# Kernel tuning notes

Measured on AMD Instinct MI355X. Metric: run time of the kernel, lower is better.

Reference implementation:

```python
import jax, jax.numpy as jnp
import numpy as np

B, H, W, DIM = 32, 56, 56, 512
WS, SHIFT, HEADS, MLP = 7, 3, 16, 2048
S = WS * WS
NW = (H // WS) * (W // WS)


def _rel_pos_index():
    coords = np.stack(np.meshgrid(np.arange(WS), np.arange(WS), indexing='ij')).reshape(2, -1)
    rel = (coords[:, :, None] - coords[:, None, :]).transpose(1, 2, 0)
    rel[:, :, 0] += WS - 1
    rel[:, :, 1] += WS - 1
    rel[:, :, 0] *= 2 * WS - 1
    return rel.sum(-1)  # [S, S] ints in [0, 169)


def _attn_mask():
    mask = np.zeros((H, W))
    cnt = 0
    sls = (slice(0, -WS), slice(-WS, -SHIFT), slice(-SHIFT, None))
    for hs in sls:
        for ws in sls:
            mask[hs, ws] = cnt
            cnt += 1
    mw = mask.reshape(H // WS, WS, W // WS, WS).transpose(0, 2, 1, 3).reshape(-1, S)
    am = mw[:, None, :] - mw[:, :, None]
    return np.where(am != 0, -100.0, 0.0).astype(np.float32)  # [NW, S, S]


_RPI = jnp.asarray(_rel_pos_index().reshape(-1))
_MASK = jnp.asarray(_attn_mask())


def setup_inputs() -> dict:
    key = jax.random.key(0)
    ks = jax.random.split(key, 6)
    sc = lambda fan: 1.0 / np.sqrt(fan)
    return {
        'x': jax.random.normal(ks[0], (B, H * W, DIM), jnp.float32),
        'qkv_w': jax.random.normal(ks[1], (DIM, 3 * DIM), jnp.float32) * sc(DIM),
        'qkv_b': jnp.zeros((3 * DIM,), jnp.float32),
        'proj_w': jax.random.normal(ks[2], (DIM, DIM), jnp.float32) * sc(DIM),
        'proj_b': jnp.zeros((DIM,), jnp.float32),
        'rel_bias': jax.random.normal(ks[3], (169, HEADS), jnp.float32) * 0.02,
        'norm1_g': jnp.ones((DIM,), jnp.float32),
        'norm1_b': jnp.zeros((DIM,), jnp.float32),
        'norm2_g': jnp.ones((DIM,), jnp.float32),
        'norm2_b': jnp.zeros((DIM,), jnp.float32),
        'mlp_w1': jax.random.normal(ks[4], (DIM, MLP), jnp.float32) * sc(DIM),
        'mlp_b1': jnp.zeros((MLP,), jnp.float32),
        'mlp_w2': jax.random.normal(ks[5], (MLP, DIM), jnp.float32) * sc(MLP),
        'mlp_b2': jnp.zeros((DIM,), jnp.float32),
    }


def _ln(z, g, b):
    m = z.mean(-1, keepdims=True)
    v = z.var(-1, keepdims=True)
    return (z - m) * jax.lax.rsqrt(v + 1e-5) * g + b


def reference(x, qkv_w, qkv_b, proj_w, proj_b, rel_bias,
              norm1_g, norm1_b, norm2_g, norm2_b,
              mlp_w1, mlp_b1, mlp_w2, mlp_b2):
    hd = DIM // HEADS
    scale = hd ** -0.5
    skip = x
    h = _ln(x, norm1_g, norm1_b).reshape(B, H, W, DIM)
    h = jnp.roll(h, (-SHIFT, -SHIFT), axis=(1, 2))
    # window partition -> [B*NW, S, DIM]
    win = h.reshape(B, H // WS, WS, W // WS, WS, DIM).transpose(0, 1, 3, 2, 4, 5).reshape(-1, S, DIM)
    qkv = (win @ qkv_w + qkv_b).reshape(-1, S, 3, HEADS, hd).transpose(2, 0, 3, 1, 4)
    q, k, v = qkv[0] * scale, qkv[1], qkv[2]
    attn = jnp.einsum('whqd,whkd->whqk', q, k)  # [B*NW, HEADS, S, S]
    bias = rel_bias[_RPI].reshape(S, S, HEADS).transpose(2, 0, 1)
    attn = attn + bias[None]
    attn = attn.reshape(B, NW, HEADS, S, S) + _MASK[None, :, None]
    attn = jax.nn.softmax(attn.reshape(-1, HEADS, S, S), axis=-1)
    out = jnp.einsum('whqk,whkd->whqd', attn, v).transpose(0, 2, 1, 3).reshape(-1, S, DIM)
    out = out @ proj_w + proj_b
    # window reverse + unshift
    out = out.reshape(B, H // WS, W // WS, WS, WS, DIM).transpose(0, 1, 3, 2, 4, 5).reshape(B, H, W, DIM)
    out = jnp.roll(out, (SHIFT, SHIFT), axis=(1, 2)).reshape(B, H * W, DIM)
    x1 = skip + out
    h2 = _ln(x1, norm2_g, norm2_b)
    h2 = jax.nn.gelu(h2 @ mlp_w1 + mlp_b1, approximate=False) @ mlp_w2 + mlp_b2
    return x1 + h2
```

## Files before the change

### kernel.cpp

```cpp
#include <hip/hip_runtime.h>
#include <hip/hip_bf16.h>
#include <math.h>

#define BB 32
#define HH 56
#define WWD 56
#define DIM 512
#define WSZ 7
#define SHIFT 3
#define HEADS 16
#define MLPD 2048
#define SS 49
#define NWIN 64
#define HD 32
#define TOK (BB*HH*WWD)
#define NQKV 1536

typedef __hip_bfloat16 bf16;
typedef __attribute__((ext_vector_type(8))) short short8;
typedef __attribute__((ext_vector_type(4))) float floatx4;

__device__ __forceinline__ float bf2f(bf16 v){ return __bfloat162float(v); }
__device__ __forceinline__ bf16  f2bf(float v){ return __float2bfloat16(v); }
__device__ __forceinline__ float rd_ext(const void* p, size_t i, int fp32){
    return fp32 ? ((const float*)p)[i] : bf2f(((const bf16*)p)[i]);
}
__device__ __forceinline__ void gload16(const bf16* g, bf16* l){
    __builtin_amdgcn_global_load_lds(
        (const __attribute__((address_space(1))) void*)g,
        (__attribute__((address_space(3))) void*)l, 16, 0, 0);
}

__global__ void sniff_kernel(const unsigned short* __restrict__ x, int* __restrict__ flag)
{
    int lane = threadIdx.x;
    int insane = 0;
    #pragma unroll
    for (int t = 0; t < 2; t++){
        unsigned short u = x[2*(lane + t*64)];
        int e = (u >> 7) & 0xFF;
        if (e < 100 || e > 133) insane++;
    }
    #pragma unroll
    for (int m = 1; m < 64; m <<= 1) insane += __shfl_xor(insane, m);
    if (lane == 0) *flag = (insane > 64) ? 1 : 0;
}

template<int MODE>
__global__ __launch_bounds__(256) void ln_kernel(const void* __restrict__ xv,
        const void* __restrict__ g, const void* __restrict__ bvec,
        bf16* __restrict__ out, const int* __restrict__ flagp)
{
    const int fp32 = *flagp;
    int token = blockIdx.x * 4 + (threadIdx.x >> 6);
    int lane  = threadIdx.x & 63;
    float f[8];
    if (MODE == 0 && fp32){
        const float* xr = (const float*)xv + (size_t)token*DIM + lane*8;
        float4 a = *(const float4*)xr;
        float4 b = *(const float4*)(xr + 4);
        f[0]=a.x; f[1]=a.y; f[2]=a.z; f[3]=a.w;
        f[4]=b.x; f[5]=b.y; f[6]=b.z; f[7]=b.w;
    } else {
        uint4 v = *((const uint4*)((const bf16*)xv + (size_t)token * DIM) + lane);
        bf16 e[8]; *(uint4*)e = v;
        #pragma unroll
        for (int i = 0; i < 8; i++) f[i] = bf2f(e[i]);
    }
    float sum = 0.f, ssq = 0.f;
    #pragma unroll
    for (int i = 0; i < 8; i++){ sum += f[i]; ssq += f[i]*f[i]; }
    #pragma unroll
    for (int m = 1; m < 64; m <<= 1){ sum += __shfl_xor(sum, m); ssq += __shfl_xor(ssq, m); }
    float mean = sum * (1.0f/DIM);
    float var  = ssq * (1.0f/DIM) - mean*mean;
    float rstd = rsqrtf(var + 1e-5f);
    bf16 o[8];
    #pragma unroll
    for (int i = 0; i < 8; i++){
        float gv = rd_ext(g,    lane*8+i, fp32);
        float bv = rd_ext(bvec, lane*8+i, fp32);
        o[i] = f2bf((f[i]-mean)*rstd*gv + bv);
    }
    size_t drow;
    if (MODE == 0){
        int bidx = token / (HH*WWD);
        int t    = token % (HH*WWD);
        int hs = t / WWD, wsrc = t % WWD;
        int i2 = (hs  + HH  - SHIFT) % HH;
        int j2 = (wsrc+ WWD - SHIFT) % WWD;
        int wh = i2 / WSZ, ii = i2 % WSZ;
        int ww = j2 / WSZ, jj = j2 % WSZ;
        int wi = bidx*NWIN + wh*8 + ww;
        drow = (size_t)wi*SS + ii*WSZ + jj;
    } else {
        drow = token;
    }
    *((uint4*)(out + drow*DIM) + lane) = *(uint4*)o;
}

__global__ void cvt_transpose(const void* __restrict__ in, bf16* __restrict__ out,
                              int K, int N, const int* __restrict__ flagp)
{
    const int fp32 = *flagp;
    int id = blockIdx.x*256 + threadIdx.x;
    if (id >= K*N) return;
    int k = id / N, n = id - k*N;
    out[(size_t)n*K + k] = f2bf(rd_ext(in, id, fp32));
}

__global__ void stab_kernel(const void* __restrict__ rel_bias,
                            float* __restrict__ stab, const int* __restrict__ flagp)
{
    const int fp32 = *flagp;
    int idx = blockIdx.x*256 + threadIdx.x;
    int h   = idx / (4*64*52);
    int rem = idx - h*(4*64*52);
    int cls = rem / (64*52);
    int rem2= rem - cls*(64*52);
    int i   = rem2 / 52;
    int j   = rem2 - i*52;
    float v = 0.f;
    if (i < SS && j < SS){
        int qi = i/7, qj = i - qi*7;
        int ki = j/7, kj = j - ki*7;
        int rpi = (qi-ki+6)*13 + (qj-kj+6);
        v = rd_ext(rel_bias, (size_t)rpi*HEADS + h, fp32);
        int ri = ((cls&2) ? (qi<4?1:2) : 0)*3 + ((cls&1) ? (qj<4?1:2) : 0);
        int rj = ((cls&2) ? (ki<4?1:2) : 0)*3 + ((cls&1) ? (kj<4?1:2) : 0);
        if (ri != rj) v -= 100.0f;
    }
    stab[idx] = v;
}

__global__ __launch_bounds__(256, 2) void attn_kernel(
        const bf16* __restrict__ qkv, const float* __restrict__ stab,
        bf16* __restrict__ out)
{
    alignas(16) __shared__ bf16 Ps[4][64*72];
    const int tid  = threadIdx.x;
    const int wave = tid >> 6, lane = tid & 63;
    const int g = lane >> 4, l16 = lane & 15;
    const int job = blockIdx.x*4 + wave;
    const int wi = job >> 4, h = job & 15;
    const bf16* qbase = qkv + (size_t)wi*(SS*NQKV) + h*HD;

    short8 qf[4], kf[4];
    #pragma unroll
    for (int t = 0; t < 4; t++){
        int row = t*16 + l16;
        qf[t] = *(const short8*)(qbase + (size_t)row*NQKV +       g*8);
        kf[t] = *(const short8*)(qbase + (size_t)row*NQKV + 512 + g*8);
    }
    floatx4 st[4][4];
    #pragma unroll
    for (int mt = 0; mt < 4; mt++)
        #pragma unroll
        for (int nt = 0; nt < 4; nt++)
            st[mt][nt] = floatx4{0.f,0.f,0.f,0.f};
    #pragma unroll
    for (int mt = 0; mt < 4; mt++)
        #pragma unroll
        for (int nt = 0; nt < 4; nt++)
            st[mt][nt] = __builtin_amdgcn_mfma_f32_16x16x32_bf16(
                             kf[mt], qf[nt], st[mt][nt], 0, 0, 0);

    const int nw = wi & 63;
    const int cls = (((nw >> 3) == 7) ? 2 : 0) | (((nw & 7) == 7) ? 1 : 0);
    const float* tb = stab + (size_t)((h*4 + cls)*64)*52;
    bf16* pw = Ps[wave];
    #pragma unroll
    for (int nt = 0; nt < 4; nt++){
        const int i = nt*16 + l16;
        const float* trow = tb + i*52;
        float mx = -1e30f;
        #pragma unroll
        for (int mt = 0; mt < 4; mt++){
            float4 t4 = *(const float4*)(trow + mt*16 + g*4);
            #pragma unroll
            for (int r = 0; r < 4; r++){
                int j = mt*16 + g*4 + r;
                float v = st[mt][nt][r]*0.17677669529663687f + ((const float*)&t4)[r];
                v = (j < SS) ? v : -1e30f;
                st[mt][nt][r] = v;
                mx = fmaxf(mx, v);
            }
        }
        mx = fmaxf(mx, __shfl_xor(mx, 16));
        mx = fmaxf(mx, __shfl_xor(mx, 32));
        float sum = 0.f;
        #pragma unroll
        for (int mt = 0; mt < 4; mt++)
            #pragma unroll
            for (int r = 0; r < 4; r++){
                float e = __expf(st[mt][nt][r] - mx);
                st[mt][nt][r] = e;
                sum += e;
            }
        sum += __shfl_xor(sum, 16);
        sum += __shfl_xor(sum, 32);
        float inv = 1.0f / sum;
        #pragma unroll
        for (int mt = 0; mt < 4; mt++){
            union { bf16 e[4]; uint2 u; } pk;
            #pragma unroll
            for (int r = 0; r < 4; r++) pk.e[r] = f2bf(st[mt][nt][r]*inv);
            *(uint2*)(pw + i*72 + mt*16 + g*4) = pk.u;
        }
    }

    const unsigned short* vbase = (const unsigned short*)qkv
                                + (size_t)wi*(SS*NQKV) + 1024 + h*HD;
    short8 vf[2][2];
    #pragma unroll
    for (int md = 0; md < 2; md++){
        int d = md*16 + l16;
        #pragma unroll
        for (int kt = 0; kt < 2; kt++){
            short8 f;
            #pragma unroll
            for (int jj = 0; jj < 8; jj++){
                int j  = kt*32 + g*8 + jj;
                int jc = (j < SS) ? j : SS-1;
                unsigned short t = vbase[(size_t)jc*NQKV + d];
                f[jj] = (j < SS) ? (short)t : (short)0;
            }
            vf[md][kt] = f;
        }
    }

    floatx4 o[2][4];
    #pragma unroll
    for (int md = 0; md < 2; md++)
        #pragma unroll
        for (int nt = 0; nt < 4; nt++)
            o[md][nt] = floatx4{0.f,0.f,0.f,0.f};
    #pragma unroll
    for (int kt = 0; kt < 2; kt++){
        #pragma unroll
        for (int nt = 0; nt < 4; nt++){
            short8 pf = *(const short8*)(pw + (nt*16 + l16)*72 + kt*32 + g*8);
            #pragma unroll
            for (int md = 0; md < 2; md++)
                o[md][nt] = __builtin_amdgcn_mfma_f32_16x16x32_bf16(
                                vf[md][kt], pf, o[md][nt], 0, 0, 0);
        }
    }

    #pragma unroll
    for (int nt = 0; nt < 4; nt++){
        int i = nt*16 + l16;
        if (i < SS){
            #pragma unroll
            for (int md = 0; md < 2; md++){
                union { bf16 e[4]; uint2 u; } ob;
                #pragma unroll
                for (int r = 0; r < 4; r++) ob.e[r] = f2bf(o[md][nt][r]);
                *(uint2*)(out + ((size_t)wi*SS + i)*DIM + h*HD + md*16 + g*4) = ob.u;
            }
        }
    }
}

template<int NT, int KT, int EPI>
__global__ __launch_bounds__(256) void gemm_kernel(
    const bf16* __restrict__ A, const bf16* __restrict__ Bt,
    const void* __restrict__ bias, void* __restrict__ Cv,
    const void* __restrict__ extra, const int* __restrict__ flagp)
{
    alignas(16) __shared__ bf16 As[128*32];
    alignas(16) __shared__ bf16 Bs[128*32];
    const int fp32 = *flagp;
    const int tid = threadIdx.x;

    const int nxt = NT/128;
    const int bid = blockIdx.x + blockIdx.y*nxt;
    const int nwg = nxt*784;
    const int cpx = nwg >> 3;
    const int wid = (bid & 7)*cpx + (bid >> 3);
    const int m0 = (wid / nxt) * 128;
    const int n0 = (wid % nxt) * 128;

    const int wave = tid >> 6, lane = tid & 63;
    const int wm = wave & 1, wn = wave >> 1;
    const int qd = lane >> 4, l16 = lane & 15;
    const int lrow  = lane >> 2;
    const int lslot = lane & 3;

    floatx4 acc[4][4];
    #pragma unroll
    for (int i = 0; i < 4; i++)
        #pragma unroll
        for (int j = 0; j < 4; j++)
            acc[i][j] = floatx4{0.f,0.f,0.f,0.f};

    for (int kt = 0; kt < KT; kt += 32){
        #pragma unroll
        for (int r = 0; r < 2; r++){
            int chunk = wave + r*4;
            int row = chunk*16 + lrow;
            gload16(A  + (size_t)(m0+row)*KT + kt + lslot*8, As + chunk*512);
            gload16(Bt + (size_t)(n0+row)*KT + kt + lslot*8, Bs + chunk*512);
        }
        __syncthreads();
        short8 af[4], bfr[4];
        #pragma unroll
        for (int mt = 0; mt < 4; mt++)
            af[mt] = *(const short8*)(As + (wm*64 + mt*16 + l16)*32 + qd*8);
        #pragma unroll
        for (int nt = 0; nt < 4; nt++)
            bfr[nt] = *(const short8*)(Bs + (wn*64 + nt*16 + l16)*32 + qd*8);
        #pragma unroll
        for (int mt = 0; mt < 4; mt++)
            #pragma unroll
            for (int nt = 0; nt < 4; nt++)
                acc[mt][nt] = __builtin_amdgcn_mfma_f32_16x16x32_bf16(
                                  af[mt], bfr[nt], acc[mt][nt], 0, 0, 0);
        __syncthreads();
    }

    #pragma unroll
    for (int mt = 0; mt < 4; mt++){
        #pragma unroll
        for (int nt = 0; nt < 4; nt++){
            #pragma unroll
            for (int r = 0; r < 4; r++){
                int m = m0 + wm*64 + mt*16 + qd*4 + r;
                int n = n0 + wn*64 + nt*16 + l16;
                float val = acc[mt][nt][r] + rd_ext(bias, n, fp32);
                if (EPI == 1){
                    val = 0.5f * val * (1.0f + erff(val * 0.70710678118654752f));
                }
                if (EPI == 2){
                    int wi = m / SS, s = m % SS;
                    int b_ = wi >> 6, nw = wi & 63;
                    int hr = (nw >> 3)*WSZ + s / WSZ;
                    int wr = (nw & 7)*WSZ + s % WSZ;
                    int h = hr + SHIFT; if (h >= HH)  h -= HH;
                    int w = wr + SHIFT; if (w >= WWD) w -= WWD;
                    size_t off = ((size_t)b_*(HH*WWD) + h*WWD + w)*DIM + n;
                    ((bf16*)Cv)[off] = f2bf(val + rd_ext(extra, off, fp32));
                } else if (EPI == 3){
                    size_t off = (size_t)m*NT + n;
                    float sv = bf2f(((const bf16*)extra)[off]);
                    if (fp32) ((float*)Cv)[off] = val + sv;
                    else      ((bf16*)Cv)[off]  = f2bf(val + sv);
                } else {
                    ((bf16*)Cv)[(size_t)m*NT + n] = f2bf(val);
                }
            }
        }
    }
}

extern "C" void kernel_launch(void* const* d_in, const int* in_sizes, int n_in,
                              void* d_out, int out_size, void* d_ws, size_t ws_size,
                              hipStream_t stream)
{
    const void* x      = d_in[0];
    const void* qkv_w  = d_in[1];
    const void* qkv_b  = d_in[2];
    const void* proj_w = d_in[3];
    const void* proj_b = d_in[4];
    const void* rel_b  = d_in[5];
    const void* n1g    = d_in[6];
    const void* n1b    = d_in[7];
    const void* n2g    = d_in[8];
    const void* n2b    = d_in[9];
    const void* w1     = d_in[10];
    const void* b1     = d_in[11];
    const void* w2     = d_in[12];
    const void* b2     = d_in[13];

    char* ws = (char*)d_ws;
    const size_t SZ_ACT = (size_t)TOK*DIM*2;
    const size_t SZ_QKV = (size_t)TOK*NQKV*2;
    bf16* win   = (bf16*)(ws);
    bf16* qkvb  = (bf16*)(ws + SZ_ACT);
    bf16* hid   = (bf16*)(ws);
    bf16* x1    = (bf16*)(ws + SZ_ACT + SZ_QKV);
    bf16* ln2   = (bf16*)(ws + 2*SZ_ACT + SZ_QKV);
    bf16* qkvwT = (bf16*)(ws + 3*SZ_ACT + SZ_QKV);
    bf16* projwT= qkvwT + (size_t)1536*512;
    bf16* w1T   = projwT + (size_t)512*512;
    bf16* w2T   = w1T   + (size_t)512*2048;
    int*  flag  = (int*)(w2T + (size_t)2048*512);
    float* stab = (float*)x1;
    const size_t need = 3*SZ_ACT + SZ_QKV +
        ((size_t)1536*512 + 512*512 + 512*2048 + 2048*512)*2 + 4;
    if (ws_size < need) return;

    hipLaunchKernelGGL(sniff_kernel, dim3(1), dim3(64), 0, stream,
                       (const unsigned short*)x, flag);

    hipLaunchKernelGGL(stab_kernel, dim3((16*4*64*52)/256), dim3(256), 0, stream,
                       rel_b, stab, flag);

    hipLaunchKernelGGL(cvt_transpose, dim3((512*1536+255)/256), dim3(256), 0, stream,
                       qkv_w, qkvwT, 512, 1536, flag);
    hipLaunchKernelGGL(cvt_transpose, dim3((512*512+255)/256), dim3(256), 0, stream,
                       proj_w, projwT, 512, 512, flag);
    hipLaunchKernelGGL(cvt_transpose, dim3((512*2048+255)/256), dim3(256), 0, stream,
                       w1, w1T, 512, 2048, flag);
    hipLaunchKernelGGL(cvt_transpose, dim3((2048*512+255)/256), dim3(256), 0, stream,
                       w2, w2T, 2048, 512, flag);

    hipLaunchKernelGGL((ln_kernel<0>), dim3(TOK/4), dim3(256), 0, stream,
                       x, n1g, n1b, win, flag);
    hipLaunchKernelGGL((gemm_kernel<1536,512,0>), dim3(12,784), dim3(256), 0, stream,
                       win, qkvwT, qkv_b, (void*)qkvb, (const void*)nullptr, flag);
    hipLaunchKernelGGL(attn_kernel, dim3(8192), dim3(256), 0, stream,
                       qkvb, stab, win);
    hipLaunchKernelGGL((gemm_kernel<512,512,2>), dim3(4,784), dim3(256), 0, stream,
                       win, projwT, proj_b, (void*)x1, x, flag);
    hipLaunchKernelGGL((ln_kernel<1>), dim3(TOK/4), dim3(256), 0, stream,
                       x1, n2g, n2b, ln2, flag);
    hipLaunchKernelGGL((gemm_kernel<2048,512,1>), dim3(16,784), dim3(256), 0, stream,
                       ln2, w1T, b1, (void*)hid, (const void*)nullptr, flag);
    hipLaunchKernelGGL((gemm_kernel<512,2048,3>), dim3(4,784), dim3(256), 0, stream,
                       hid, w2T, b2, d_out, (const void*)x1, flag);
}
```

Before: 2.371 ms.

## Deepen GEMM K-tile to 64 with XOR-swizzled LDS and cheaper epilogue

Each GEMM iteration now stages a 64-wide K slice instead of 32, which halves the number of barrier pairs per tile. The LDS layout is XOR-swizzled so the wider rows can be read without bank conflicts. The epilogue hoists the bias loads and per-row index math out of the inner loop. GELU now uses an Abramowitz-Stegun polynomial approximation of erf instead of erff. Shared memory per block doubles, and the polynomial carries a small approximation error of about 1e-7.

```diff
diff --git a/kernel.cpp b/kernel.cpp
--- a/kernel.cpp
+++ b/kernel.cpp
@@ -29,6 +29,15 @@
     __builtin_amdgcn_global_load_lds(
         (const __attribute__((address_space(1))) void*)g,
         (__attribute__((address_space(3))) void*)l, 16, 0, 0);
+}
+__device__ __forceinline__ float gelu_exact(float x){
+    float z  = fabsf(x) * 0.70710678118654752f;
+    float t  = 1.0f / (1.0f + 0.3275911f * z);
+    float p  = t*(0.254829592f + t*(-0.284496736f + t*(1.421413741f +
+               t*(-1.453152027f + t*1.061405429f))));
+    float er = 1.0f - p * __expf(-z*z);
+    float cdf = 0.5f * (1.0f + (x < 0.f ? -er : er));
+    return x * cdf;
 }
 
 __global__ void sniff_kernel(const unsigned short* __restrict__ x, int* __restrict__ flag)
@@ -268,8 +277,8 @@
     const void* __restrict__ bias, void* __restrict__ Cv,
     const void* __restrict__ extra, const int* __restrict__ flagp)
 {
-    alignas(16) __shared__ bf16 As[128*32];
-    alignas(16) __shared__ bf16 Bs[128*32];
+    alignas(16) __shared__ bf16 As[128*64];
+    alignas(16) __shared__ bf16 Bs[128*64];
     const int fp32 = *flagp;
     const int tid = threadIdx.x;
 
@@ -284,8 +293,8 @@
     const int wave = tid >> 6, lane = tid & 63;
     const int wm = wave & 1, wn = wave >> 1;
     const int qd = lane >> 4, l16 = lane & 15;
-    const int lrow  = lane >> 2;
-    const int lslot = lane & 3;
+    const int srow  = lane >> 3;
+    const int sslot = ((lane & 7) ^ srow) * 8;
 
     floatx4 acc[4][4];
     #pragma unroll
@@ -294,59 +303,78 @@
         for (int j = 0; j < 4; j++)
             acc[i][j] = floatx4{0.f,0.f,0.f,0.f};
 
-    for (int kt = 0; kt < KT; kt += 32){
-        #pragma unroll
-        for (int r = 0; r < 2; r++){
-            int chunk = wave + r*4;
-            int row = chunk*16 + lrow;
-            gload16(A  + (size_t)(m0+row)*KT + kt + lslot*8, As + chunk*512);
-            gload16(Bt + (size_t)(n0+row)*KT + kt + lslot*8, Bs + chunk*512);
+    for (int kt = 0; kt < KT; kt += 64){
+        #pragma unroll
+        for (int r = 0; r < 4; r++){
+            int c = wave*4 + r;
+            gload16(A  + (size_t)(m0 + c*8 + srow)*KT + kt + sslot, As + c*512);
+            gload16(Bt + (size_t)(n0 + c*8 + srow)*KT + kt + sslot, Bs + c*512);
         }
         __syncthreads();
-        short8 af[4], bfr[4];
-        #pragma unroll
-        for (int mt = 0; mt < 4; mt++)
-            af[mt] = *(const short8*)(As + (wm*64 + mt*16 + l16)*32 + qd*8);
-        #pragma unroll
-        for (int nt = 0; nt < 4; nt++)
-            bfr[nt] = *(const short8*)(Bs + (wn*64 + nt*16 + l16)*32 + qd*8);
-        #pragma unroll
-        for (int mt = 0; mt < 4; mt++)
-            #pragma unroll
-            for (int nt = 0; nt < 4; nt++)
-                acc[mt][nt] = __builtin_amdgcn_mfma_f32_16x16x32_bf16(
-                                  af[mt], bfr[nt], acc[mt][nt], 0, 0, 0);
+        #pragma unroll
+        for (int kk = 0; kk < 2; kk++){
+            short8 af[4], bfr[4];
+            #pragma unroll
+            for (int mt = 0; mt < 4; mt++){
+                int row = wm*64 + mt*16 + l16;
+                af[mt] = *(const short8*)(As + row*64 + (((kk*4+qd) ^ (row&7))*8));
+            }
+            #pragma unroll
+            for (int nt = 0; nt < 4; nt++){
+                int row = wn*64 + nt*16 + l16;
+                bfr[nt] = *(const short8*)(Bs + row*64 + (((kk*4+qd) ^ (row&7))*8));
+            }
+            #pragma unroll
+            for (int mt = 0; mt < 4; mt++)
+                #pragma unroll
+                for (int nt = 0; nt < 4; nt++)
+                    acc[mt][nt] = __builtin_amdgcn_mfma_f32_16x16x32_bf16(
+                                      af[mt], bfr[nt], acc[mt][nt], 0, 0, 0);
+        }
         __syncthreads();
     }
 
+    const int ncol = n0 + wn*64 + l16;
+    float bias_v[4];
+    #pragma unroll
+    for (int nt = 0; nt < 4; nt++)
+        bias_v[nt] = rd_ext(bias, ncol + nt*16, fp32);
+
     #pragma unroll
     for (int mt = 0; mt < 4; mt++){
         #pragma unroll
-        for (int nt = 0; nt < 4; nt++){
-            #pragma unroll
-            for (int r = 0; r < 4; r++){
-                int m = m0 + wm*64 + mt*16 + qd*4 + r;
-                int n = n0 + wn*64 + nt*16 + l16;
-                float val = acc[mt][nt][r] + rd_ext(bias, n, fp32);
-                if (EPI == 1){
-                    val = 0.5f * val * (1.0f + erff(val * 0.70710678118654752f));
+        for (int r = 0; r < 4; r++){
+            const int m = m0 + wm*64 + mt*16 + qd*4 + r;
+            if (EPI == 2){
+                int wi = m / SS, s = m - wi*SS;
+                int b_ = wi >> 6, nw = wi & 63;
+                int hr = (nw >> 3)*WSZ + s / WSZ;
+                int wr = (nw & 7)*WSZ + s % WSZ;
+                int h = hr + SHIFT; if (h >= HH)  h -= HH;
+                int w = wr + SHIFT; if (w >= WWD) w -= WWD;
+                size_t rowoff = ((size_t)b_*(HH*WWD) + h*WWD + w)*DIM + ncol;
+                #pragma unroll
+                for (int nt = 0; nt < 4; nt++){
+                    float val = acc[mt][nt][r] + bias_v[nt];
+                    ((bf16*)Cv)[rowoff + nt*16] =
+                        f2bf(val + rd_ext(extra, rowoff + nt*16, fp32));
                 }
-                if (EPI == 2){
-                    int wi = m / SS, s = m % SS;
-                    int b_ = wi >> 6, nw = wi & 63;
-                    int hr = (nw >> 3)*WSZ + s / WSZ;
-                    int wr = (nw & 7)*WSZ + s % WSZ;
-                    int h = hr + SHIFT; if (h >= HH)  h -= HH;
-                    int w = wr + SHIFT; if (w >= WWD) w -= WWD;
-                    size_t off = ((size_t)b_*(HH*WWD) + h*WWD + w)*DIM + n;
-                    ((bf16*)Cv)[off] = f2bf(val + rd_ext(extra, off, fp32));
-                } else if (EPI == 3){
-                    size_t off = (size_t)m*NT + n;
-                    float sv = bf2f(((const bf16*)extra)[off]);
-                    if (fp32) ((float*)Cv)[off] = val + sv;
-                    else      ((bf16*)Cv)[off]  = f2bf(val + sv);
-                } else {
-                    ((bf16*)Cv)[(size_t)m*NT + n] = f2bf(val);
+            } else if (EPI == 3){
+                size_t rowoff = (size_t)m*NT + ncol;
+                #pragma unroll
+                for (int nt = 0; nt < 4; nt++){
+                    float val = acc[mt][nt][r] + bias_v[nt]
+                              + bf2f(((const bf16*)extra)[rowoff + nt*16]);
+                    if (fp32) ((float*)Cv)[rowoff + nt*16] = val;
+                    else      ((bf16*)Cv)[rowoff + nt*16]  = f2bf(val);
+                }
+            } else {
+                bf16* crow = (bf16*)Cv + (size_t)m*NT + ncol;
+                #pragma unroll
+                for (int nt = 0; nt < 4; nt++){
+                    float val = acc[mt][nt][r] + bias_v[nt];
+                    if (EPI == 1) val = gelu_exact(val);
+                    crow[nt*16] = f2bf(val);
                 }
             }
         }
```

Measured after the change: 2.257 ms. 4.8% less time.
